# Kernel tuning notes

Hardware: AMD Instinct MI355X
Metric: run time of the kernel (lower is better)

## Reference

```python
import jax, jax.numpy as jnp
import numpy as np

D_HIDDEN = 1024
NUM_HEADS = 16
D_HEAD = D_HIDDEN // NUM_HEADS


def setup_inputs() -> dict:
    key = jax.random.key(0)
    ks = jax.random.split(key, 9)
    N, S, D = 4, 2048, D_HIDDEN
    s = 1.0 / np.sqrt(D)
    inp = {
        "x": jax.random.normal(ks[0], (N, S, D), dtype=jnp.float32),
        "Wq": jax.random.uniform(ks[1], (D, D), jnp.float32, -s, s),
        "bq": jnp.zeros((D,), jnp.float32),
        "Wk": jax.random.uniform(ks[2], (D, D), jnp.float32, -s, s),
        "bk": jnp.zeros((D,), jnp.float32),
        "Wv": jax.random.uniform(ks[3], (D, D), jnp.float32, -s, s),
        "bv": jnp.zeros((D,), jnp.float32),
        "Wo": jax.random.uniform(ks[4], (D, D), jnp.float32, -s, s),
        "bo": jnp.zeros((D,), jnp.float32),
        "ln_gamma": jnp.ones((D,), jnp.float32),
        "ln_beta": jnp.zeros((D,), jnp.float32),
    }
    return inp


def _layer_norm(x, gamma, beta, eps=1e-5):
    mu = jnp.mean(x, axis=-1, keepdims=True)
    var = jnp.var(x, axis=-1, keepdims=True)
    return (x - mu) * jax.lax.rsqrt(var + eps) * gamma + beta


def reference(x, Wq, bq, Wk, bk, Wv, bv, Wo, bo, ln_gamma, ln_beta):
    N, S, D = x.shape
    H, Dh = NUM_HEADS, D_HEAD
    xn = _layer_norm(x, ln_gamma, ln_beta)
    # torch Linear: y = x @ W.T + b
    q = (xn @ Wq.T + bq).reshape(N, S, H, Dh)
    k = (xn @ Wk.T + bk).reshape(N, S, H, Dh)
    v = (xn @ Wv.T + bv).reshape(N, S, H, Dh)
    # scores: [N, H, S, S]
    scores = jnp.einsum('nxhd,nyhd->nhxy', q, k) / np.sqrt(Dh)
    # causal mask: positions y > x get -inf
    mask = jnp.triu(jnp.full((S, S), -jnp.inf, dtype=scores.dtype), k=1)
    attn = jax.nn.softmax(scores + mask[None, None], axis=-1)
    z = jnp.einsum('nhxy,nyhd->nxhd', attn, v).reshape(N, S, D)
    return z @ Wo.T + bo
```

## Files before the change

kernel.cpp:

```cpp
#include <hip/hip_runtime.h>

typedef unsigned short u16;
typedef unsigned int   u32;
typedef __bf16 bf16x8 __attribute__((ext_vector_type(8)));
typedef float  f32x4  __attribute__((ext_vector_type(4)));
typedef unsigned short u16x8 __attribute__((ext_vector_type(8)));
typedef unsigned short u16x4 __attribute__((ext_vector_type(4)));

#define SEQ 2048
#define DM  1024
#define TOKS 8388608
#define SCLQ 0.18033688f

__device__ __forceinline__ float bf2f(u16 u) {
    u32 i = ((u32)u) << 16;
    float f; __builtin_memcpy(&f, &i, 4); return f;
}
__device__ __forceinline__ u16 f2bf(float f) {
    u32 i; __builtin_memcpy(&i, &f, 4);
    return (u16)((i + 0x7FFFu + ((i >> 16) & 1u)) >> 16);
}
__device__ __forceinline__ bf16x8 ld8(const u16* p) {
    return __builtin_bit_cast(bf16x8, *(const u16x8*)p);
}
#define GLD16(src, dst) __builtin_amdgcn_global_load_lds( \
    (const __attribute__((address_space(1))) void*)(src), \
    (__attribute__((address_space(3))) void*)(dst), 16, 0, 0)

__device__ __forceinline__ int sniff_fp32(const u32* x) {
    u32 w = x[threadIdx.x & 63];
    int e0 = (int)((w >> 7) & 0xFFu);
    int cnt = (e0 >= 100 && e0 <= 140) ? 1 : 0;
#pragma unroll
    for (int off = 32; off; off >>= 1) cnt += __shfl_xor(cnt, off);
    return cnt < 32;
}

__global__ __launch_bounds__(256) void prep_k(const void* __restrict__ x,
                                              const void* Wq, const void* Wk, const void* Wv, const void* Wo,
                                              const void* bq, const void* bk, const void* bv, const void* bo,
                                              const void* g, const void* b,
                                              u16* __restrict__ dstW, u16* __restrict__ dstV,
                                              u16* __restrict__ xn, int* __restrict__ flagp) {
    const int bid = blockIdx.x, tid = threadIdx.x;
    const int fp32m = sniff_fp32((const u32*)x);

    if (bid < 8192) {
        const int row = bid;
        float f[4], s1 = 0.f, s2 = 0.f;
        if (fp32m) {
            f32x4 v = *(const f32x4*)((const float*)x + (size_t)row * DM + tid * 4);
#pragma unroll
            for (int j = 0; j < 4; ++j) f[j] = v[j];
        } else {
            u16x4 v = *(const u16x4*)((const u16*)x + (size_t)row * DM + tid * 4);
#pragma unroll
            for (int j = 0; j < 4; ++j) f[j] = bf2f(v[j]);
        }
#pragma unroll
        for (int j = 0; j < 4; ++j) { s1 += f[j]; s2 += f[j] * f[j]; }
#pragma unroll
        for (int off = 32; off; off >>= 1) { s1 += __shfl_xor(s1, off); s2 += __shfl_xor(s2, off); }
        __shared__ float red[8];
        const int wave = tid >> 6, lane = tid & 63;
        if (lane == 0) { red[wave] = s1; red[4 + wave] = s2; }
        __syncthreads();
        s1 = red[0] + red[1] + red[2] + red[3];
        s2 = red[4] + red[5] + red[6] + red[7];
        const float mu = s1 * (1.f / DM);
        const float var = s2 * (1.f / DM) - mu * mu;
        const float rs = rsqrtf(var + 1e-5f);
        float gv[4], bv2[4];
        if (fp32m) {
            f32x4 gg = *(const f32x4*)((const float*)g + tid * 4);
            f32x4 bb = *(const f32x4*)((const float*)b + tid * 4);
#pragma unroll
            for (int j = 0; j < 4; ++j) { gv[j] = gg[j]; bv2[j] = bb[j]; }
        } else {
            u16x4 gg = *(const u16x4*)((const u16*)g + tid * 4);
            u16x4 bb = *(const u16x4*)((const u16*)b + tid * 4);
#pragma unroll
            for (int j = 0; j < 4; ++j) { gv[j] = bf2f(gg[j]); bv2[j] = bf2f(bb[j]); }
        }
        u16x4 o;
#pragma unroll
        for (int j = 0; j < 4; ++j) o[j] = f2bf((f[j] - mu) * rs * gv[j] + bv2[j]);
        *(u16x4*)(xn + (size_t)row * DM + tid * 4) = o;
    } else if (bid < 12288) {
        if (!fp32m) return;
        const int wi = (bid - 8192) >> 10, blk = (bid - 8192) & 1023;
        const void* src = (wi == 0) ? Wq : (wi == 1) ? Wk : (wi == 2) ? Wv : Wo;
        const size_t off = (size_t)blk * 1024 + tid * 4;
        const float* f = (const float*)src + off;
        u16x4 o;
#pragma unroll
        for (int j = 0; j < 4; ++j) o[j] = f2bf(f[j]);
        *(u16x4*)(dstW + (size_t)wi * 1048576 + off) = o;
    } else {
#pragma unroll
        for (int i = 0; i < 4; ++i) {
            const void* src = (i == 0) ? bq : (i == 1) ? bk : (i == 2) ? bv : bo;
            u16x4 o;
            if (fp32m) {
                const float* f = (const float*)src + tid * 4;
#pragma unroll
                for (int j = 0; j < 4; ++j) o[j] = f2bf(f[j]);
            } else {
                o = *(const u16x4*)((const u16*)src + tid * 4);
            }
            *(u16x4*)(dstV + (size_t)i * 1024 + tid * 4) = o;
        }
        if (tid == 0) *flagp = fp32m;
    }
}

template <int VT>
__device__ __forceinline__ void gemm_core(u16* As, u16* Bs,
                                          const u16* __restrict__ A,
                                          const u16* __restrict__ W,
                                          const u16* __restrict__ bias,
                                          u16* __restrict__ out,
                                          float scale) {
    const int tid = threadIdx.x, wave = tid >> 6, lane = tid & 63;
    const int l4 = lane & 15, q4 = lane >> 4;
    const int bm = blockIdx.x, bn = blockIdx.y;
    const int wm = (wave >> 1) * 64, wn = (wave & 1) * 64;
    f32x4 acc[4][4] = {};
    const int srow = wave * 32 + (lane >> 2);
    const int skoff = (lane & 3) * 8;
    const u16* Ag = A + ((size_t)(bm * 128 + srow)) * DM + skoff;
    const u16* Wg = W + ((size_t)(bn * 128 + srow)) * DM + skoff;
    u16* As0 = As + wave * 1024;
    u16* Bs0 = Bs + wave * 1024;

    for (int k0 = 0; k0 < DM; k0 += 32) {
        GLD16(Ag + k0, As0);
        GLD16(Ag + 16 * DM + k0, As0 + 512);
        GLD16(Wg + k0, Bs0);
        GLD16(Wg + 16 * DM + k0, Bs0 + 512);
        __syncthreads();
        bf16x8 af[4], bfr[4];
#pragma unroll
        for (int t = 0; t < 4; ++t)
            af[t] = ld8(As + (wm + t * 16 + l4) * 32 + q4 * 8);
#pragma unroll
        for (int t = 0; t < 4; ++t)
            bfr[t] = ld8(Bs + (wn + t * 16 + l4) * 32 + q4 * 8);
#pragma unroll
        for (int mt = 0; mt < 4; ++mt)
#pragma unroll
            for (int nt = 0; nt < 4; ++nt)
                acc[mt][nt] = __builtin_amdgcn_mfma_f32_16x16x32_bf16(af[mt], bfr[nt], acc[mt][nt], 0, 0, 0);
        __syncthreads();
    }

#pragma unroll
    for (int nt = 0; nt < 4; ++nt) {
        const int col = bn * 128 + wn + nt * 16 + l4;
        const float bs = bf2f(bias[col]);
#pragma unroll
        for (int mt = 0; mt < 4; ++mt) {
            const int row0 = bm * 128 + wm + mt * 16 + q4 * 4;
            if (VT == 1) {
                const int nb = row0 >> 11, s0 = row0 & 2047;
                u16x4 pk;
#pragma unroll
                for (int r = 0; r < 4; ++r) pk[r] = f2bf((acc[mt][nt][r] + bs) * scale);
                *(u16x4*)(out + ((size_t)(nb * 1024 + col)) * SEQ + s0) = pk;
            } else {
#pragma unroll
                for (int r = 0; r < 4; ++r)
                    out[(size_t)(row0 + r) * DM + col] = f2bf((acc[mt][nt][r] + bs) * scale);
            }
        }
    }
}

__global__ __launch_bounds__(256) void gemm_qkv_k(const u16* __restrict__ xn, const u16* __restrict__ Wc,
                                                  const u16* __restrict__ Vc,
                                                  const void* Wq, const void* Wk, const void* Wv,
                                                  const int* __restrict__ flagp,
                                                  u16* __restrict__ Q, u16* __restrict__ K, u16* __restrict__ Vt) {
    __shared__ alignas(16) u16 As[128 * 32];
    __shared__ alignas(16) u16 Bs[128 * 32];
    const int z = blockIdx.z;
    const int fp32m = *flagp;
    if (z == 0) {
        const u16* W = fp32m ? Wc : (const u16*)Wq;
        gemm_core<0>(As, Bs, xn, W, Vc, Q, SCLQ);
    } else if (z == 1) {
        const u16* W = fp32m ? (Wc + 1048576) : (const u16*)Wk;
        gemm_core<0>(As, Bs, xn, W, Vc + 1024, K, 1.0f);
    } else {
        const u16* W = fp32m ? (Wc + 2 * 1048576) : (const u16*)Wv;
        gemm_core<1>(As, Bs, xn, W, Vc + 2048, Vt, 1.0f);
    }
}

__global__ __launch_bounds__(512) void gemm_out_k(const u16* __restrict__ Z, const u16* __restrict__ Wc,
                                                  const u16* __restrict__ Vc, const void* Wo,
                                                  u16* __restrict__ out, const int* __restrict__ flagp) {
    __shared__ alignas(16) u16 As[128 * 32];
    __shared__ alignas(16) u16 Bs[128 * 32];
    const int fp32m = *flagp;
    const u16* W = fp32m ? (Wc + 3 * 1048576) : (const u16*)Wo;
    const u16* bias = Vc + 3 * 1024;
    const int tid = threadIdx.x, wave = tid >> 6, lane = tid & 63;
    const int l4 = lane & 15, q4 = lane >> 4;
    const int bm = blockIdx.x, bn = blockIdx.y;
    const int wm = (wave >> 2) * 64, wn = (wave & 3) * 32;
    f32x4 acc[4][2] = {};
    const int srow = (wave & 3) * 32 + (lane >> 2);
    const int skoff = (lane & 3) * 8;
    const u16* Sg = (wave < 4) ? (Z + ((size_t)(bm * 128 + srow)) * DM + skoff)
                               : (W + ((size_t)(bn * 128 + srow)) * DM + skoff);
    u16* dst0 = (wave < 4) ? (As + (wave & 3) * 1024) : (Bs + (wave & 3) * 1024);

    for (int k0 = 0; k0 < DM; k0 += 32) {
        GLD16(Sg + k0, dst0);
        GLD16(Sg + 16 * DM + k0, dst0 + 512);
        __syncthreads();
        bf16x8 af[4], bfr[2];
#pragma unroll
        for (int t = 0; t < 4; ++t)
            af[t] = ld8(As + (wm + t * 16 + l4) * 32 + q4 * 8);
#pragma unroll
        for (int t = 0; t < 2; ++t)
            bfr[t] = ld8(Bs + (wn + t * 16 + l4) * 32 + q4 * 8);
#pragma unroll
        for (int mt = 0; mt < 4; ++mt)
#pragma unroll
            for (int nt = 0; nt < 2; ++nt)
                acc[mt][nt] = __builtin_amdgcn_mfma_f32_16x16x32_bf16(af[mt], bfr[nt], acc[mt][nt], 0, 0, 0);
        __syncthreads();
    }

#pragma unroll
    for (int nt = 0; nt < 2; ++nt) {
        const int col = bn * 128 + wn + nt * 16 + l4;
        const float bs = bf2f(bias[col]);
#pragma unroll
        for (int mt = 0; mt < 4; ++mt) {
            const int row0 = bm * 128 + wm + mt * 16 + q4 * 4;
            if (fp32m) {
#pragma unroll
                for (int r = 0; r < 4; ++r)
                    ((float*)out)[(size_t)(row0 + r) * DM + col] = acc[mt][nt][r] + bs;
            } else {
#pragma unroll
                for (int r = 0; r < 4; ++r)
                    out[(size_t)(row0 + r) * DM + col] = f2bf(acc[mt][nt][r] + bs);
            }
        }
    }
}

__global__ __launch_bounds__(256, 2) void flash_k(const u16* __restrict__ Q,
                                                  const u16* __restrict__ K,
                                                  const u16* __restrict__ Vt,
                                                  u16* __restrict__ Z) {
    const int bh = blockIdx.x;
    const int yy = (int)blockIdx.y;
    const int qb = (yy < 4) ? yy : 11 - yy;
    const int n = bh >> 4, h = bh & 15;
    const int tid = threadIdx.x, wave = tid >> 6, lane = tid & 63;
    const int l4 = lane & 15, q4 = lane >> 4;

    __shared__ alignas(16) u16 Ks[2][64 * 32];
    __shared__ alignas(16) u16 Vs[2][64 * 32];
    __shared__ alignas(16) u16 Pl[4][4][16 * 72];

    const int Q0w = qb * 256 + wave * 64;
    bf16x8 qf[4][2];
#pragma unroll
    for (int qt = 0; qt < 4; ++qt) {
        const u16* Qr = Q + ((size_t)(n * SEQ + Q0w + qt * 16 + l4)) * DM + h * 64 + q4 * 8;
        qf[qt][0] = ld8(Qr);
        qf[qt][1] = ld8(Qr + 32);
    }

    const int srow = lane >> 2, scol = (lane & 3) * 8;
    const u16* Kg = K + ((size_t)(n * SEQ + wave * 16 + srow)) * DM + h * 64 + scol;
    const u16* Vg = Vt + ((size_t)(n * 1024 + h * 64 + wave * 16 + srow)) * SEQ + scol;
    u16* KsD0 = &Ks[0][wave * 512];
    u16* KsD1 = &Ks[1][wave * 512];
    u16* VsD0 = &Vs[0][wave * 512];
    u16* VsD1 = &Vs[1][wave * 512];

    f32x4 o[4][4] = {};
    float l_acc[4] = {0.f, 0.f, 0.f, 0.f};
    const int nch = 4 * qb + 4;

    for (int c = 0; c < nch; ++c) {
        const int kv0 = c * 64;
        const size_t krow = (size_t)kv0 * DM;
        GLD16(Kg + krow, KsD0);
        GLD16(Kg + krow + 32, KsD1);
        GLD16(Vg + kv0, VsD0);
        GLD16(Vg + kv0 + 32, VsD1);
        __syncthreads();

        bf16x8 a[4][2];
#pragma unroll
        for (int mt = 0; mt < 4; ++mt) {
            a[mt][0] = ld8(&Ks[0][(mt * 16 + l4) * 32 + q4 * 8]);
            a[mt][1] = ld8(&Ks[1][(mt * 16 + l4) * 32 + q4 * 8]);
        }
#pragma unroll
        for (int qt = 0; qt < 4; ++qt) {
            const int qbase = Q0w + qt * 16;
            if (kv0 > qbase + 15) continue;
            f32x4 st[4];
#pragma unroll
            for (int mt = 0; mt < 4; ++mt) {
                f32x4 zz = {0.f, 0.f, 0.f, 0.f};
                st[mt] = __builtin_amdgcn_mfma_f32_16x16x32_bf16(a[mt][0], qf[qt][0], zz, 0, 0, 0);
                st[mt] = __builtin_amdgcn_mfma_f32_16x16x32_bf16(a[mt][1], qf[qt][1], st[mt], 0, 0, 0);
            }
            u16* P = Pl[wave][qt];
            float la = l_acc[qt];
            if (kv0 + 63 <= qbase) {
#pragma unroll
                for (int mt = 0; mt < 4; ++mt) {
                    __bf16 pk[4];
#pragma unroll
                    for (int r = 0; r < 4; ++r) {
                        float p = __builtin_amdgcn_exp2f(st[mt][r]);
                        la += p;
                        pk[r] = (__bf16)p;
                    }
                    *(u16x4*)(P + l4 * 72 + mt * 16 + q4 * 4) = *(u16x4*)pk;
                }
            } else {
                const int qg = qbase + l4;
#pragma unroll
                for (int mt = 0; mt < 4; ++mt) {
                    __bf16 pk[4];
#pragma unroll
                    for (int r = 0; r < 4; ++r) {
                        const int kv = kv0 + mt * 16 + q4 * 4 + r;
                        float p = __builtin_amdgcn_exp2f(st[mt][r]);
                        p = (kv > qg) ? 0.f : p;
                        la += p;
                        pk[r] = (__bf16)p;
                    }
                    *(u16x4*)(P + l4 * 72 + mt * 16 + q4 * 4) = *(u16x4*)pk;
                }
            }
            l_acc[qt] = la;
        }
#pragma unroll
        for (int ks = 0; ks < 2; ++ks) {
            bf16x8 vf[4];
#pragma unroll
            for (int nt = 0; nt < 4; ++nt)
                vf[nt] = ld8(&Vs[ks][(nt * 16 + l4) * 32 + q4 * 8]);
#pragma unroll
            for (int qt = 0; qt < 4; ++qt) {
                if (kv0 > Q0w + qt * 16 + 15) continue;
                bf16x8 pf = ld8(&Pl[wave][qt][l4 * 72 + ks * 32 + q4 * 8]);
#pragma unroll
                for (int nt = 0; nt < 4; ++nt)
                    o[qt][nt] = __builtin_amdgcn_mfma_f32_16x16x32_bf16(pf, vf[nt], o[qt][nt], 0, 0, 0);
            }
        }
        __syncthreads();
    }

#pragma unroll
    for (int qt = 0; qt < 4; ++qt) {
        float l = l_acc[qt];
        l += __shfl_xor(l, 16);
        l += __shfl_xor(l, 32);
        float lr[4];
#pragma unroll
        for (int r = 0; r < 4; ++r) lr[r] = 1.f / __shfl(l, q4 * 4 + r);
#pragma unroll
        for (int nt = 0; nt < 4; ++nt) {
            const int col = h * 64 + nt * 16 + l4;
#pragma unroll
            for (int r = 0; r < 4; ++r) {
                const int row = n * SEQ + Q0w + qt * 16 + q4 * 4 + r;
                Z[(size_t)row * DM + col] = f2bf(o[qt][nt][r] * lr[r]);
            }
        }
    }
}

extern "C" void kernel_launch(void* const* d_in, const int* in_sizes, int n_in,
                              void* d_out, int out_size, void* d_ws, size_t ws_size,
                              hipStream_t stream) {
    const void* x  = d_in[0];
    const void* Wq = d_in[1];
    const void* bq = d_in[2];
    const void* Wk = d_in[3];
    const void* bk = d_in[4];
    const void* Wv = d_in[5];
    const void* bv = d_in[6];
    const void* Wo = d_in[7];
    const void* bo = d_in[8];
    const void* g  = d_in[9];
    const void* b  = d_in[10];
    u16* ws = (u16*)d_ws;

    u16* xn  = ws;
    u16* Qb  = ws + (size_t)TOKS;
    u16* Kb  = ws + (size_t)2 * TOKS;
    u16* Vtb = ws + (size_t)3 * TOKS;
    u16* Zb  = ws;
    u16* Wc  = ws + (size_t)4 * TOKS;
    u16* Vc  = Wc + 4 * 1048576;
    int* flagp = (int*)(Vc + 8 * 1024);

    prep_k<<<dim3(12289), 256, 0, stream>>>(x, Wq, Wk, Wv, Wo, bq, bk, bv, bo, g, b, Wc, Vc, xn, flagp);
    gemm_qkv_k<<<dim3(64, 8, 3), 256, 0, stream>>>(xn, Wc, Vc, Wq, Wk, Wv, flagp, Qb, Kb, Vtb);
    flash_k<<<dim3(64, 8), 256, 0, stream>>>(Qb, Kb, Vtb, Zb);
    gemm_out_k<<<dim3(64, 8), 512, 0, stream>>>(Zb, Wc, Vc, Wo, (u16*)d_out, flagp);
}
```

Measured before the change: 275.4 us.

## Pair complementary 128-row query tiles per block for causal load balance

The attention kernel now uses 128-row query tiles, 32 rows per wave, instead of 256-row tiles. Each block processes two tiles, 15-y and y, so every block handles the same number of KV chunks under the causal mask. This removes the tail imbalance where some blocks did far more chunks than others. In exchange each staged K/V chunk feeds half as many query rows, which roughly doubles total K/V shared-memory traffic and syncs.

```diff
diff --git a/kernel.cpp b/kernel.cpp
--- a/kernel.cpp
+++ b/kernel.cpp
@@ -255,25 +255,20 @@
     }
 }
 
-__global__ __launch_bounds__(256, 2) void flash_k(const u16* __restrict__ Q,
-                                                  const u16* __restrict__ K,
-                                                  const u16* __restrict__ Vt,
-                                                  u16* __restrict__ Z) {
-    const int bh = blockIdx.x;
-    const int yy = (int)blockIdx.y;
-    const int qb = (yy < 4) ? yy : 11 - yy;
-    const int n = bh >> 4, h = bh & 15;
+__device__ __forceinline__ void flash_tile(int n, int h, int qb,
+                                           const u16* __restrict__ Q,
+                                           const u16* __restrict__ K,
+                                           const u16* __restrict__ Vt,
+                                           u16* __restrict__ Z,
+                                           u16* Ks0, u16* Ks1, u16* Vs0, u16* Vs1,
+                                           u16* P0, u16* P1) {
     const int tid = threadIdx.x, wave = tid >> 6, lane = tid & 63;
     const int l4 = lane & 15, q4 = lane >> 4;
 
-    __shared__ alignas(16) u16 Ks[2][64 * 32];
-    __shared__ alignas(16) u16 Vs[2][64 * 32];
-    __shared__ alignas(16) u16 Pl[4][4][16 * 72];
-
-    const int Q0w = qb * 256 + wave * 64;
-    bf16x8 qf[4][2];
-#pragma unroll
-    for (int qt = 0; qt < 4; ++qt) {
+    const int Q0w = qb * 128 + wave * 32;
+    bf16x8 qf[2][2];
+#pragma unroll
+    for (int qt = 0; qt < 2; ++qt) {
         const u16* Qr = Q + ((size_t)(n * SEQ + Q0w + qt * 16 + l4)) * DM + h * 64 + q4 * 8;
         qf[qt][0] = ld8(Qr);
         qf[qt][1] = ld8(Qr + 32);
@@ -282,14 +277,14 @@
     const int srow = lane >> 2, scol = (lane & 3) * 8;
     const u16* Kg = K + ((size_t)(n * SEQ + wave * 16 + srow)) * DM + h * 64 + scol;
     const u16* Vg = Vt + ((size_t)(n * 1024 + h * 64 + wave * 16 + srow)) * SEQ + scol;
-    u16* KsD0 = &Ks[0][wave * 512];
-    u16* KsD1 = &Ks[1][wave * 512];
-    u16* VsD0 = &Vs[0][wave * 512];
-    u16* VsD1 = &Vs[1][wave * 512];
-
-    f32x4 o[4][4] = {};
-    float l_acc[4] = {0.f, 0.f, 0.f, 0.f};
-    const int nch = 4 * qb + 4;
+    u16* KsD0 = Ks0 + wave * 512;
+    u16* KsD1 = Ks1 + wave * 512;
+    u16* VsD0 = Vs0 + wave * 512;
+    u16* VsD1 = Vs1 + wave * 512;
+
+    f32x4 o[2][4] = {};
+    float l_acc[2] = {0.f, 0.f};
+    const int nch = 2 * qb + 2;
 
     for (int c = 0; c < nch; ++c) {
         const int kv0 = c * 64;
@@ -303,11 +298,11 @@
         bf16x8 a[4][2];
 #pragma unroll
         for (int mt = 0; mt < 4; ++mt) {
-            a[mt][0] = ld8(&Ks[0][(mt * 16 + l4) * 32 + q4 * 8]);
-            a[mt][1] = ld8(&Ks[1][(mt * 16 + l4) * 32 + q4 * 8]);
-        }
-#pragma unroll
-        for (int qt = 0; qt < 4; ++qt) {
+            a[mt][0] = ld8(Ks0 + (mt * 16 + l4) * 32 + q4 * 8);
+            a[mt][1] = ld8(Ks1 + (mt * 16 + l4) * 32 + q4 * 8);
+        }
+#pragma unroll
+        for (int qt = 0; qt < 2; ++qt) {
             const int qbase = Q0w + qt * 16;
             if (kv0 > qbase + 15) continue;
             f32x4 st[4];
@@ -317,7 +312,7 @@
                 st[mt] = __builtin_amdgcn_mfma_f32_16x16x32_bf16(a[mt][0], qf[qt][0], zz, 0, 0, 0);
                 st[mt] = __builtin_amdgcn_mfma_f32_16x16x32_bf16(a[mt][1], qf[qt][1], st[mt], 0, 0, 0);
             }
-            u16* P = Pl[wave][qt];
+            u16* P = qt ? P1 : P0;
             float la = l_acc[qt];
             if (kv0 + 63 <= qbase) {
 #pragma unroll
@@ -354,21 +349,22 @@
             bf16x8 vf[4];
 #pragma unroll
             for (int nt = 0; nt < 4; ++nt)
-                vf[nt] = ld8(&Vs[ks][(nt * 16 + l4) * 32 + q4 * 8]);
-#pragma unroll
-            for (int qt = 0; qt < 4; ++qt) {
-                if (kv0 > Q0w + qt * 16 + 15) continue;
-                bf16x8 pf = ld8(&Pl[wave][qt][l4 * 72 + ks * 32 + q4 * 8]);
-#pragma unroll
-                for (int nt = 0; nt < 4; ++nt)
-                    o[qt][nt] = __builtin_amdgcn_mfma_f32_16x16x32_bf16(pf, vf[nt], o[qt][nt], 0, 0, 0);
-            }
-        }
-        __syncthreads();
-    }
-
-#pragma unroll
-    for (int qt = 0; qt < 4; ++qt) {
+                vf[nt] = ld8((ks ? Vs1 : Vs0) + (nt * 16 + l4) * 32 + q4 * 8);
+            bf16x8 pf0 = ld8(P0 + l4 * 72 + ks * 32 + q4 * 8);
+            bf16x8 pf1 = ld8(P1 + l4 * 72 + ks * 32 + q4 * 8);
+#pragma unroll
+            for (int nt = 0; nt < 4; ++nt) {
+                if (kv0 <= Q0w + 15)
+                    o[0][nt] = __builtin_amdgcn_mfma_f32_16x16x32_bf16(pf0, vf[nt], o[0][nt], 0, 0, 0);
+                if (kv0 <= Q0w + 31)
+                    o[1][nt] = __builtin_amdgcn_mfma_f32_16x16x32_bf16(pf1, vf[nt], o[1][nt], 0, 0, 0);
+            }
+        }
+        __syncthreads();
+    }
+
+#pragma unroll
+    for (int qt = 0; qt < 2; ++qt) {
         float l = l_acc[qt];
         l += __shfl_xor(l, 16);
         l += __shfl_xor(l, 32);
@@ -385,6 +381,22 @@
             }
         }
     }
+}
+
+__global__ __launch_bounds__(256, 2) void flash_k(const u16* __restrict__ Q,
+                                                  const u16* __restrict__ K,
+                                                  const u16* __restrict__ Vt,
+                                                  u16* __restrict__ Z) {
+    const int bh = blockIdx.x, y = blockIdx.y;
+    const int n = bh >> 4, h = bh & 15;
+    const int wave = threadIdx.x >> 6;
+
+    __shared__ alignas(16) u16 Ks[2][64 * 32];
+    __shared__ alignas(16) u16 Vs[2][64 * 32];
+    __shared__ alignas(16) u16 Pl[4][2][16 * 72];
+
+    flash_tile(n, h, 15 - y, Q, K, Vt, Z, Ks[0], Ks[1], Vs[0], Vs[1], Pl[wave][0], Pl[wave][1]);
+    flash_tile(n, h, y,      Q, K, Vt, Z, Ks[0], Ks[1], Vs[0], Vs[1], Pl[wave][0], Pl[wave][1]);
 }
 
 extern "C" void kernel_launch(void* const* d_in, const int* in_sizes, int n_in,
```

New measurement: 260.0 us. 5.6% less time.
